# Kernel tuning notes

Hardware: AMD Instinct MI355X
Metric: run time of the kernel (lower is better)

## Reference

```python
import jax, jax.numpy as jnp
import numpy as np

B, T, D, H, OUT = 1024, 512, 64, 32, 2
EPS = 1e-5

def setup_inputs() -> dict:
    key = jax.random.key(0)
    ks = jax.random.split(key, 16)
    s_ih1 = 1.0 / np.sqrt(H)
    inp = {
        'x': jax.random.normal(ks[0], (B, T, D), jnp.float32),
        'bn_gamma': jax.random.normal(ks[1], (T,), jnp.float32) * 0.1 + 1.0,
        'bn_beta': jax.random.normal(ks[2], (T,), jnp.float32) * 0.1,
        'bn_mean': jax.random.normal(ks[3], (T,), jnp.float32) * 0.1,
        'bn_var': jax.random.uniform(ks[4], (T,), jnp.float32) + 0.5,
        'Wih1': jax.random.uniform(ks[5], (4 * H, D), jnp.float32, -s_ih1, s_ih1),
        'Whh1': jax.random.uniform(ks[6], (4 * H, H), jnp.float32, -s_ih1, s_ih1),
        'bih1': jax.random.uniform(ks[7], (4 * H,), jnp.float32, -s_ih1, s_ih1),
        'bhh1': jax.random.uniform(ks[8], (4 * H,), jnp.float32, -s_ih1, s_ih1),
        'Wih2': jax.random.uniform(ks[9], (4 * H, H), jnp.float32, -s_ih1, s_ih1),
        'Whh2': jax.random.uniform(ks[10], (4 * H, H), jnp.float32, -s_ih1, s_ih1),
        'bih2': jax.random.uniform(ks[11], (4 * H,), jnp.float32, -s_ih1, s_ih1),
        'bhh2': jax.random.uniform(ks[12], (4 * H,), jnp.float32, -s_ih1, s_ih1),
        'fcW': jax.random.uniform(ks[13], (OUT, H), jnp.float32, -s_ih1, s_ih1),
        'fcb': jax.random.uniform(ks[14], (OUT,), jnp.float32, -s_ih1, s_ih1),
    }
    return inp

def _lstm_layer(x, Wih, Whh, bih, bhh):
    # x: (B, T, Din) -> outputs h_t for all t: (B, T, H)
    h = jnp.shape(Whh)[1]
    # precompute input contributions for all timesteps: (B, T, 4H)
    xw = jnp.einsum('btd,gd->btg', x, Wih) + bih + bhh
    def step(carry, xt):
        h_prev, c_prev = carry
        z = xt + h_prev @ Whh.T  # (B, 4H)
        i = jax.nn.sigmoid(z[:, :h])
        f = jax.nn.sigmoid(z[:, h:2 * h])
        g = jnp.tanh(z[:, 2 * h:3 * h])
        o = jax.nn.sigmoid(z[:, 3 * h:])
        c = f * c_prev + i * g
        hn = o * jnp.tanh(c)
        return (hn, c), hn
    b = x.shape[0]
    init = (jnp.zeros((b, h), x.dtype), jnp.zeros((b, h), x.dtype))
    _, hs = jax.lax.scan(step, init, jnp.swapaxes(xw, 0, 1))  # (T, B, H)
    return jnp.swapaxes(hs, 0, 1)

def reference(x, bn_gamma, bn_beta, bn_mean, bn_var,
              Wih1, Whh1, bih1, bhh1, Wih2, Whh2, bih2, bhh2, fcW, fcb):
    # BatchNorm1d over channel dim=1 (axis_num), eval mode (running stats);
    # dropout layers are identity in eval mode.
    inv = jax.lax.rsqrt(bn_var + EPS)
    xn = (x - bn_mean[None, :, None]) * (inv * bn_gamma)[None, :, None] + bn_beta[None, :, None]
    h1 = _lstm_layer(xn, Wih1, Whh1, bih1, bhh1)   # (B, T, 32)
    h2 = _lstm_layer(h1, Wih2, Whh2, bih2, bhh2)   # (B, T, 32)
    pooled = h2.mean(axis=-2)                       # GAP over time: (B, 32)
    return pooled @ fcW.T + fcb                     # (B, 2)
```

## Files before the change

kernel.cpp:

```cpp
#include <hip/hip_runtime.h>
#include <cstdint>

#define B_   1024
#define T_   512
#define D_   64
#define H_   32
#define EPS_ 1e-5f

__device__ __forceinline__ float fast_rcp(float x) { return __builtin_amdgcn_rcpf(x); }

__global__ __launch_bounds__(256, 3) void k_bnxw(
    const float* __restrict__ x,   const float* __restrict__ gam,
    const float* __restrict__ bet, const float* __restrict__ mu,
    const float* __restrict__ var,
    const float* __restrict__ Wih1, const float* __restrict__ bih1,
    const float* __restrict__ bhh1, float* __restrict__ pre)
{
    __shared__ __align__(16) float Wt[64][132];
    __shared__ __align__(16) float xs[64][64];
    __shared__ float scs[64], shs[64], bsum[128];

    const int tid = threadIdx.x;
    const int r0  = blockIdx.x * 64;

    if (tid < 64) {
        int t = (r0 + tid) & (T_ - 1);
        float s = rsqrtf(var[t] + EPS_) * gam[t];
        scs[tid] = s;
        shs[tid] = bet[t] - mu[t] * s;
    }
    if (tid >= 128) bsum[tid - 128] = bih1[tid - 128] + bhh1[tid - 128];

    #pragma unroll
    for (int it = 0; it < 8; ++it) {
        int idx4 = tid + it * 256;
        float4 v = ((const float4*)Wih1)[idx4];
        int g  = idx4 >> 4;
        int k0 = (idx4 & 15) * 4;
        Wt[k0 + 0][g] = v.x; Wt[k0 + 1][g] = v.y;
        Wt[k0 + 2][g] = v.z; Wt[k0 + 3][g] = v.w;
    }
    __syncthreads();

    const float4* x4 = (const float4*)(x + (size_t)r0 * 64);
    #pragma unroll
    for (int it = 0; it < 4; ++it) {
        int j  = tid + it * 256;
        int rr = j >> 4;
        int k4 = j & 15;
        float4 v = x4[j];
        float s = scs[rr], sh = shs[rr];
        v.x = v.x * s + sh; v.y = v.y * s + sh;
        v.z = v.z * s + sh; v.w = v.w * s + sh;
        *(float4*)&xs[rr][k4 * 4] = v;
    }
    __syncthreads();

    const int gq = tid & 31;
    const int rq = tid >> 5;

    float acc[8][4];
    #pragma unroll
    for (int r = 0; r < 8; ++r)
        #pragma unroll
        for (int q = 0; q < 4; ++q) acc[r][q] = 0.f;

    #pragma unroll 4
    for (int kq = 0; kq < 16; ++kq) {
        float4 wv[4];
        #pragma unroll
        for (int kk = 0; kk < 4; ++kk)
            wv[kk] = *(const float4*)&Wt[kq * 4 + kk][gq * 4];
        #pragma unroll
        for (int rr = 0; rr < 8; ++rr) {
            float4 xv = *(const float4*)&xs[rq * 8 + rr][kq * 4];
            acc[rr][0] += xv.x * wv[0].x + xv.y * wv[1].x + xv.z * wv[2].x + xv.w * wv[3].x;
            acc[rr][1] += xv.x * wv[0].y + xv.y * wv[1].y + xv.z * wv[2].y + xv.w * wv[3].y;
            acc[rr][2] += xv.x * wv[0].z + xv.y * wv[1].z + xv.z * wv[2].z + xv.w * wv[3].z;
            acc[rr][3] += xv.x * wv[0].w + xv.y * wv[1].w + xv.z * wv[2].w + xv.w * wv[3].w;
        }
    }

    const float b0 = bsum[gq * 4 + 0], b1 = bsum[gq * 4 + 1];
    const float b2 = bsum[gq * 4 + 2], b3 = bsum[gq * 4 + 3];
    #pragma unroll
    for (int rr = 0; rr < 8; ++rr) {
        int row = r0 + rq * 8 + rr;
        float4 o = make_float4(acc[rr][0] + b0, acc[rr][1] + b1,
                               acc[rr][2] + b2, acc[rr][3] + b3);
        *(float4*)&pre[(size_t)row * 128 + gq * 4] = o;
    }
}

__global__ __launch_bounds__(256, 4) void k_rec(
    const float* __restrict__ pre,
    const float* __restrict__ Whh1, const float* __restrict__ Wih2,
    const float* __restrict__ Whh2, const float* __restrict__ bih2,
    const float* __restrict__ bhh2, const float* __restrict__ fcW,
    const float* __restrict__ fcb,  float* __restrict__ out)
{
    __shared__ __align__(16) float h1s[2][H_];
    __shared__ __align__(16) float h2s[2][H_];
    __shared__ float zw[4][32];
    __shared__ float pool[H_];

    const int tid  = threadIdx.x;
    const int w    = tid >> 6;
    const int l    = tid & 63;
    const int m    = l >> 1;
    const int half = l & 1;
    const int jj   = m & 7;
    const int q    = m >> 3;
    const int g    = w * 8 + jj + 32 * q;
    const int b    = blockIdx.x;

    if (tid < H_) { h1s[0][tid] = 0.f; h2s[0][tid] = 0.f; }

    float w1h[16], wi2h[16], w2h[16];
    {
        const float4* p4 = (const float4*)(Whh1 + g * 32 + half * 16);
        #pragma unroll
        for (int i = 0; i < 4; ++i) {
            float4 v = p4[i];
            w1h[4*i] = v.x; w1h[4*i+1] = v.y; w1h[4*i+2] = v.z; w1h[4*i+3] = v.w;
        }
    }
    {
        const float4* p4 = (const float4*)(Wih2 + g * 32 + half * 16);
        #pragma unroll
        for (int i = 0; i < 4; ++i) {
            float4 v = p4[i];
            wi2h[4*i] = v.x; wi2h[4*i+1] = v.y; wi2h[4*i+2] = v.z; wi2h[4*i+3] = v.w;
        }
    }
    {
        const float4* p4 = (const float4*)(Whh2 + g * 32 + half * 16);
        #pragma unroll
        for (int i = 0; i < 4; ++i) {
            float4 v = p4[i];
            w2h[4*i] = v.x; w2h[4*i+1] = v.y; w2h[4*i+2] = v.z; w2h[4*i+3] = v.w;
        }
    }
    #pragma unroll
    for (int i = 0; i < 16; ++i) {
        asm volatile("" : "+v"(w1h[i]));
        asm volatile("" : "+v"(wi2h[i]));
        asm volatile("" : "+v"(w2h[i]));
    }
    float bias1 = (half == 0) ? 0.f : 0.f;
    float bias2 = (half == 0) ? (bih2[g] + bhh2[g]) : 0.f;
    asm volatile("" : "+v"(bias2));
    (void)bias1;

    const float act_a = (q == 2) ? 2.f : 1.f;
    const float act_b = (q == 2) ? -1.f : 0.f;

    __syncthreads();

    const float* prow = pre + (size_t)b * T_ * 128;
    float zc = prow[g];
    float c1 = 0.f, c2 = 0.f, hsum = 0.f;
    const bool wrH = (half == 0) && (q == 0);

    for (int t = 0; t < T_; ++t) {
        const int p = t & 1;

        float zn = 0.f;
        if (t + 1 < T_) zn = prow[(size_t)(t + 1) * 128 + g];

        {
            const float* h1p = &h1s[p][half * 16];
            float a0 = (half == 0) ? zc : 0.f;
            float a1 = 0.f, a2 = 0.f, a3 = 0.f;
            #pragma unroll
            for (int i = 0; i < 4; ++i) {
                float4 v = *(const float4*)(h1p + 4 * i);
                a0 += w1h[4*i]   * v.x; a1 += w1h[4*i+1] * v.y;
                a2 += w1h[4*i+2] * v.z; a3 += w1h[4*i+3] * v.w;
            }
            float za = (a0 + a1) + (a2 + a3);
            za += __shfl_xor(za, 1);

            float u = act_a * za;
            float s = fast_rcp(1.f + __expf(-u));
            float act = fmaf(act_a, s, act_b);
            if (half == 0) zw[w][m] = act;
            float i_ = zw[w][jj],      f_ = zw[w][jj + 8];
            float g_ = zw[w][jj + 16], o_ = zw[w][jj + 24];
            c1 = f_ * c1 + i_ * g_;
            float th = fmaf(2.f, fast_rcp(1.f + __expf(-2.f * c1)), -1.f);
            float h1 = o_ * th;
            if (wrH) h1s[1 - p][w * 8 + jj] = h1;
        }

        __syncthreads();

        {
            const float* h1n = &h1s[1 - p][half * 16];
            const float* h2p = &h2s[p][half * 16];
            float s0 = bias2, s1 = 0.f, s2 = 0.f, s3 = 0.f;
            #pragma unroll
            for (int i = 0; i < 4; ++i) {
                float4 v = *(const float4*)(h1n + 4 * i);
                s0 += wi2h[4*i]   * v.x; s1 += wi2h[4*i+1] * v.y;
                s2 += wi2h[4*i+2] * v.z; s3 += wi2h[4*i+3] * v.w;
            }
            #pragma unroll
            for (int i = 0; i < 4; ++i) {
                float4 v = *(const float4*)(h2p + 4 * i);
                s0 += w2h[4*i]   * v.x; s1 += w2h[4*i+1] * v.y;
                s2 += w2h[4*i+2] * v.z; s3 += w2h[4*i+3] * v.w;
            }
            float zb = (s0 + s1) + (s2 + s3);
            zb += __shfl_xor(zb, 1);

            float u = act_a * zb;
            float s = fast_rcp(1.f + __expf(-u));
            float act = fmaf(act_a, s, act_b);
            if (half == 0) zw[w][m] = act;
            float i_ = zw[w][jj],      f_ = zw[w][jj + 8];
            float g_ = zw[w][jj + 16], o_ = zw[w][jj + 24];
            c2 = f_ * c2 + i_ * g_;
            float th = fmaf(2.f, fast_rcp(1.f + __expf(-2.f * c2)), -1.f);
            float h2v = o_ * th;
            hsum += h2v;
            if (wrH) h2s[1 - p][w * 8 + jj] = h2v;
        }
        zc = zn;
    }

    if (wrH) pool[w * 8 + jj] = hsum * (1.f / T_);
    __syncthreads();
    if (tid < 2) {
        float acc = fcb[tid];
        #pragma unroll
        for (int j = 0; j < 32; ++j) acc += pool[j] * fcW[tid * 32 + j];
        out[b * 2 + tid] = acc;
    }
}

extern "C" void kernel_launch(void* const* d_in, const int* in_sizes, int n_in,
                              void* d_out, int out_size, void* d_ws, size_t ws_size,
                              hipStream_t stream)
{
    const float* x    = (const float*)d_in[0];
    const float* gam  = (const float*)d_in[1];
    const float* bet  = (const float*)d_in[2];
    const float* mu   = (const float*)d_in[3];
    const float* var  = (const float*)d_in[4];
    const float* Wih1 = (const float*)d_in[5];
    const float* Whh1 = (const float*)d_in[6];
    const float* bih1 = (const float*)d_in[7];
    const float* bhh1 = (const float*)d_in[8];
    const float* Wih2 = (const float*)d_in[9];
    const float* Whh2 = (const float*)d_in[10];
    const float* bih2 = (const float*)d_in[11];
    const float* bhh2 = (const float*)d_in[12];
    const float* fcW  = (const float*)d_in[13];
    const float* fcb  = (const float*)d_in[14];
    float*       out  = (float*)d_out;

    float* pre = (float*)d_ws;

    k_bnxw<<<dim3(B_ * T_ / 64), 256, 0, stream>>>(
        x, gam, bet, mu, var, Wih1, bih1, bhh1, pre);
    k_rec<<<dim3(B_), 256, 0, stream>>>(
        pre, Whh1, Wih2, Whh2, bih2, bhh2, fcW, fcb, out);
}
```

Baseline: 747.2 us.

## Remap LSTM recurrence to one gate per thread with DPP quad exchange

The recurrent kernel drops from 256 to 128 threads per block. Each thread now computes a full 32-wide dot product for one gate instead of half of one, which removes the xor-shuffle reduction. The four gates of a cell now sit in adjacent lanes of a quad and are exchanged with DPP quad permutes instead of a shared-memory zw buffer. The time loop is unrolled by two, with prefetch two steps ahead. Separately, the input-projection kernel doubles its row tile to 128 rows per block, raising accumulator register pressure and lowering occupancy.

```diff
diff --git a/kernel.cpp b/kernel.cpp
--- a/kernel.cpp
+++ b/kernel.cpp
@@ -7,9 +7,16 @@
 #define H_   32
 #define EPS_ 1e-5f
 
-__device__ __forceinline__ float fast_rcp(float x) { return __builtin_amdgcn_rcpf(x); }
-
-__global__ __launch_bounds__(256, 3) void k_bnxw(
+__device__ __forceinline__ float rcp_(float x) { return __builtin_amdgcn_rcpf(x); }
+
+template<int CTRL>
+__device__ __forceinline__ float qperm(float x) {
+    int i = __builtin_bit_cast(int, x);
+    i = __builtin_amdgcn_mov_dpp(i, CTRL, 0xF, 0xF, true);
+    return __builtin_bit_cast(float, i);
+}
+
+__global__ __launch_bounds__(256, 2) void k_bnxw(
     const float* __restrict__ x,   const float* __restrict__ gam,
     const float* __restrict__ bet, const float* __restrict__ mu,
     const float* __restrict__ var,
@@ -17,41 +24,42 @@
     const float* __restrict__ bhh1, float* __restrict__ pre)
 {
     __shared__ __align__(16) float Wt[64][132];
-    __shared__ __align__(16) float xs[64][64];
-    __shared__ float scs[64], shs[64], bsum[128];
+    __shared__ __align__(16) float xs[128][64];
+    __shared__ float scs[128], shs[128], bsum[128];
 
     const int tid = threadIdx.x;
-    const int r0  = blockIdx.x * 64;
-
-    if (tid < 64) {
+    const int r0  = blockIdx.x * 128;
+
+    if (tid < 128) {
         int t = (r0 + tid) & (T_ - 1);
         float s = rsqrtf(var[t] + EPS_) * gam[t];
         scs[tid] = s;
         shs[tid] = bet[t] - mu[t] * s;
-    }
-    if (tid >= 128) bsum[tid - 128] = bih1[tid - 128] + bhh1[tid - 128];
+    } else {
+        bsum[tid - 128] = bih1[tid - 128] + bhh1[tid - 128];
+    }
 
     #pragma unroll
     for (int it = 0; it < 8; ++it) {
         int idx4 = tid + it * 256;
         float4 v = ((const float4*)Wih1)[idx4];
-        int g  = idx4 >> 4;
+        int gg = idx4 >> 4;
         int k0 = (idx4 & 15) * 4;
-        Wt[k0 + 0][g] = v.x; Wt[k0 + 1][g] = v.y;
-        Wt[k0 + 2][g] = v.z; Wt[k0 + 3][g] = v.w;
+        Wt[k0 + 0][gg] = v.x; Wt[k0 + 1][gg] = v.y;
+        Wt[k0 + 2][gg] = v.z; Wt[k0 + 3][gg] = v.w;
     }
     __syncthreads();
 
     const float4* x4 = (const float4*)(x + (size_t)r0 * 64);
     #pragma unroll
-    for (int it = 0; it < 4; ++it) {
+    for (int it = 0; it < 8; ++it) {
         int j  = tid + it * 256;
         int rr = j >> 4;
         int k4 = j & 15;
         float4 v = x4[j];
         float s = scs[rr], sh = shs[rr];
-        v.x = v.x * s + sh; v.y = v.y * s + sh;
-        v.z = v.z * s + sh; v.w = v.w * s + sh;
+        v.x = fmaf(v.x, s, sh); v.y = fmaf(v.y, s, sh);
+        v.z = fmaf(v.z, s, sh); v.w = fmaf(v.w, s, sh);
         *(float4*)&xs[rr][k4 * 4] = v;
     }
     __syncthreads();
@@ -59,40 +67,52 @@
     const int gq = tid & 31;
     const int rq = tid >> 5;
 
-    float acc[8][4];
-    #pragma unroll
-    for (int r = 0; r < 8; ++r)
-        #pragma unroll
-        for (int q = 0; q < 4; ++q) acc[r][q] = 0.f;
-
-    #pragma unroll 4
+    float acc[16][4];
+    #pragma unroll
+    for (int r = 0; r < 16; ++r)
+        #pragma unroll
+        for (int c = 0; c < 4; ++c) acc[r][c] = 0.f;
+
+    #pragma unroll 2
     for (int kq = 0; kq < 16; ++kq) {
-        float4 wv[4];
-        #pragma unroll
-        for (int kk = 0; kk < 4; ++kk)
-            wv[kk] = *(const float4*)&Wt[kq * 4 + kk][gq * 4];
-        #pragma unroll
-        for (int rr = 0; rr < 8; ++rr) {
-            float4 xv = *(const float4*)&xs[rq * 8 + rr][kq * 4];
-            acc[rr][0] += xv.x * wv[0].x + xv.y * wv[1].x + xv.z * wv[2].x + xv.w * wv[3].x;
-            acc[rr][1] += xv.x * wv[0].y + xv.y * wv[1].y + xv.z * wv[2].y + xv.w * wv[3].y;
-            acc[rr][2] += xv.x * wv[0].z + xv.y * wv[1].z + xv.z * wv[2].z + xv.w * wv[3].z;
-            acc[rr][3] += xv.x * wv[0].w + xv.y * wv[1].w + xv.z * wv[2].w + xv.w * wv[3].w;
+        float4 wv0 = *(const float4*)&Wt[kq * 4 + 0][gq * 4];
+        float4 wv1 = *(const float4*)&Wt[kq * 4 + 1][gq * 4];
+        float4 wv2 = *(const float4*)&Wt[kq * 4 + 2][gq * 4];
+        float4 wv3 = *(const float4*)&Wt[kq * 4 + 3][gq * 4];
+        #pragma unroll
+        for (int rr = 0; rr < 16; ++rr) {
+            float4 xv = *(const float4*)&xs[rq * 16 + rr][kq * 4];
+            acc[rr][0] = fmaf(xv.x, wv0.x, acc[rr][0]);
+            acc[rr][0] = fmaf(xv.y, wv1.x, acc[rr][0]);
+            acc[rr][0] = fmaf(xv.z, wv2.x, acc[rr][0]);
+            acc[rr][0] = fmaf(xv.w, wv3.x, acc[rr][0]);
+            acc[rr][1] = fmaf(xv.x, wv0.y, acc[rr][1]);
+            acc[rr][1] = fmaf(xv.y, wv1.y, acc[rr][1]);
+            acc[rr][1] = fmaf(xv.z, wv2.y, acc[rr][1]);
+            acc[rr][1] = fmaf(xv.w, wv3.y, acc[rr][1]);
+            acc[rr][2] = fmaf(xv.x, wv0.z, acc[rr][2]);
+            acc[rr][2] = fmaf(xv.y, wv1.z, acc[rr][2]);
+            acc[rr][2] = fmaf(xv.z, wv2.z, acc[rr][2]);
+            acc[rr][2] = fmaf(xv.w, wv3.z, acc[rr][2]);
+            acc[rr][3] = fmaf(xv.x, wv0.w, acc[rr][3]);
+            acc[rr][3] = fmaf(xv.y, wv1.w, acc[rr][3]);
+            acc[rr][3] = fmaf(xv.z, wv2.w, acc[rr][3]);
+            acc[rr][3] = fmaf(xv.w, wv3.w, acc[rr][3]);
         }
     }
 
     const float b0 = bsum[gq * 4 + 0], b1 = bsum[gq * 4 + 1];
     const float b2 = bsum[gq * 4 + 2], b3 = bsum[gq * 4 + 3];
     #pragma unroll
-    for (int rr = 0; rr < 8; ++rr) {
-        int row = r0 + rq * 8 + rr;
+    for (int rr = 0; rr < 16; ++rr) {
+        int row = r0 + rq * 16 + rr;
         float4 o = make_float4(acc[rr][0] + b0, acc[rr][1] + b1,
                                acc[rr][2] + b2, acc[rr][3] + b3);
         *(float4*)&pre[(size_t)row * 128 + gq * 4] = o;
     }
 }
 
-__global__ __launch_bounds__(256, 4) void k_rec(
+__global__ __launch_bounds__(128, 2) void k_rec(
     const float* __restrict__ pre,
     const float* __restrict__ Whh1, const float* __restrict__ Wih2,
     const float* __restrict__ Whh2, const float* __restrict__ bih2,
@@ -101,135 +121,118 @@
 {
     __shared__ __align__(16) float h1s[2][H_];
     __shared__ __align__(16) float h2s[2][H_];
-    __shared__ float zw[4][32];
     __shared__ float pool[H_];
 
     const int tid  = threadIdx.x;
     const int w    = tid >> 6;
     const int l    = tid & 63;
-    const int m    = l >> 1;
-    const int half = l & 1;
-    const int jj   = m & 7;
-    const int q    = m >> 3;
-    const int g    = w * 8 + jj + 32 * q;
+    const int jj   = l >> 2;
+    const int q    = l & 3;
+    const int g    = w * 16 + jj + 32 * q;
+    const int cell = w * 16 + jj;
+    const bool q0  = (q == 0);
     const int b    = blockIdx.x;
 
     if (tid < H_) { h1s[0][tid] = 0.f; h2s[0][tid] = 0.f; }
 
-    float w1h[16], wi2h[16], w2h[16];
+    float w1[32], wi2[32], w2h[32];
     {
-        const float4* p4 = (const float4*)(Whh1 + g * 32 + half * 16);
-        #pragma unroll
-        for (int i = 0; i < 4; ++i) {
+        const float4* p4 = (const float4*)(Whh1 + g * 32);
+        #pragma unroll
+        for (int i = 0; i < 8; ++i) {
             float4 v = p4[i];
-            w1h[4*i] = v.x; w1h[4*i+1] = v.y; w1h[4*i+2] = v.z; w1h[4*i+3] = v.w;
+            w1[4*i] = v.x; w1[4*i+1] = v.y; w1[4*i+2] = v.z; w1[4*i+3] = v.w;
         }
     }
     {
-        const float4* p4 = (const float4*)(Wih2 + g * 32 + half * 16);
-        #pragma unroll
-        for (int i = 0; i < 4; ++i) {
+        const float4* p4 = (const float4*)(Wih2 + g * 32);
+        #pragma unroll
+        for (int i = 0; i < 8; ++i) {
             float4 v = p4[i];
-            wi2h[4*i] = v.x; wi2h[4*i+1] = v.y; wi2h[4*i+2] = v.z; wi2h[4*i+3] = v.w;
+            wi2[4*i] = v.x; wi2[4*i+1] = v.y; wi2[4*i+2] = v.z; wi2[4*i+3] = v.w;
         }
     }
     {
-        const float4* p4 = (const float4*)(Whh2 + g * 32 + half * 16);
-        #pragma unroll
-        for (int i = 0; i < 4; ++i) {
+        const float4* p4 = (const float4*)(Whh2 + g * 32);
+        #pragma unroll
+        for (int i = 0; i < 8; ++i) {
             float4 v = p4[i];
             w2h[4*i] = v.x; w2h[4*i+1] = v.y; w2h[4*i+2] = v.z; w2h[4*i+3] = v.w;
         }
     }
-    #pragma unroll
-    for (int i = 0; i < 16; ++i) {
-        asm volatile("" : "+v"(w1h[i]));
-        asm volatile("" : "+v"(wi2h[i]));
-        asm volatile("" : "+v"(w2h[i]));
-    }
-    float bias1 = (half == 0) ? 0.f : 0.f;
-    float bias2 = (half == 0) ? (bih2[g] + bhh2[g]) : 0.f;
-    asm volatile("" : "+v"(bias2));
-    (void)bias1;
+    const float bias2 = bih2[g] + bhh2[g];
 
     const float act_a = (q == 2) ? 2.f : 1.f;
     const float act_b = (q == 2) ? -1.f : 0.f;
-
-    __syncthreads();
-
-    const float* prow = pre + (size_t)b * T_ * 128;
-    float zc = prow[g];
+    const float nact  = -act_a;
+
+    __syncthreads();
+
+    const float* prow = pre + (size_t)b * T_ * 128 + g;
+    float zc = prow[0];
+    float zn = prow[128];
     float c1 = 0.f, c2 = 0.f, hsum = 0.f;
-    const bool wrH = (half == 0) && (q == 0);
-
-    for (int t = 0; t < T_; ++t) {
-        const int p = t & 1;
-
-        float zn = 0.f;
-        if (t + 1 < T_) zn = prow[(size_t)(t + 1) * 128 + g];
-
-        {
-            const float* h1p = &h1s[p][half * 16];
-            float a0 = (half == 0) ? zc : 0.f;
-            float a1 = 0.f, a2 = 0.f, a3 = 0.f;
-            #pragma unroll
-            for (int i = 0; i < 4; ++i) {
-                float4 v = *(const float4*)(h1p + 4 * i);
-                a0 += w1h[4*i]   * v.x; a1 += w1h[4*i+1] * v.y;
-                a2 += w1h[4*i+2] * v.z; a3 += w1h[4*i+3] * v.w;
-            }
-            float za = (a0 + a1) + (a2 + a3);
-            za += __shfl_xor(za, 1);
-
-            float u = act_a * za;
-            float s = fast_rcp(1.f + __expf(-u));
-            float act = fmaf(act_a, s, act_b);
-            if (half == 0) zw[w][m] = act;
-            float i_ = zw[w][jj],      f_ = zw[w][jj + 8];
-            float g_ = zw[w][jj + 16], o_ = zw[w][jj + 24];
-            c1 = f_ * c1 + i_ * g_;
-            float th = fmaf(2.f, fast_rcp(1.f + __expf(-2.f * c1)), -1.f);
-            float h1 = o_ * th;
-            if (wrH) h1s[1 - p][w * 8 + jj] = h1;
-        }
-
-        __syncthreads();
-
-        {
-            const float* h1n = &h1s[1 - p][half * 16];
-            const float* h2p = &h2s[p][half * 16];
-            float s0 = bias2, s1 = 0.f, s2 = 0.f, s3 = 0.f;
-            #pragma unroll
-            for (int i = 0; i < 4; ++i) {
-                float4 v = *(const float4*)(h1n + 4 * i);
-                s0 += wi2h[4*i]   * v.x; s1 += wi2h[4*i+1] * v.y;
-                s2 += wi2h[4*i+2] * v.z; s3 += wi2h[4*i+3] * v.w;
-            }
-            #pragma unroll
-            for (int i = 0; i < 4; ++i) {
-                float4 v = *(const float4*)(h2p + 4 * i);
-                s0 += w2h[4*i]   * v.x; s1 += w2h[4*i+1] * v.y;
-                s2 += w2h[4*i+2] * v.z; s3 += w2h[4*i+3] * v.w;
-            }
-            float zb = (s0 + s1) + (s2 + s3);
-            zb += __shfl_xor(zb, 1);
-
-            float u = act_a * zb;
-            float s = fast_rcp(1.f + __expf(-u));
-            float act = fmaf(act_a, s, act_b);
-            if (half == 0) zw[w][m] = act;
-            float i_ = zw[w][jj],      f_ = zw[w][jj + 8];
-            float g_ = zw[w][jj + 16], o_ = zw[w][jj + 24];
-            c2 = f_ * c2 + i_ * g_;
-            float th = fmaf(2.f, fast_rcp(1.f + __expf(-2.f * c2)), -1.f);
-            float h2v = o_ * th;
-            hsum += h2v;
-            if (wrH) h2s[1 - p][w * 8 + jj] = h2v;
-        }
-        zc = zn;
-    }
-
-    if (wrH) pool[w * 8 + jj] = hsum * (1.f / T_);
+
+#define STEP(P, ZIN)                                                          \
+    {                                                                         \
+        const float4* h1p = (const float4*)&h1s[P][0];                        \
+        float a0 = (ZIN), a1 = 0.f, a2 = 0.f, a3 = 0.f;                       \
+        _Pragma("unroll")                                                     \
+        for (int i = 0; i < 8; ++i) {                                         \
+            float4 v = h1p[i];                                                \
+            a0 = fmaf(w1[4*i+0], v.x, a0); a1 = fmaf(w1[4*i+1], v.y, a1);     \
+            a2 = fmaf(w1[4*i+2], v.z, a2); a3 = fmaf(w1[4*i+3], v.w, a3);     \
+        }                                                                     \
+        float z1 = (a0 + a1) + (a2 + a3);                                     \
+        float A1 = fmaf(act_a, rcp_(1.f + __expf(nact * z1)), act_b);         \
+        float B1 = qperm<0xB1>(A1);                                           \
+        float C1 = qperm<0x4E>(A1);                                           \
+        float D1 = qperm<0x1B>(A1);                                           \
+        c1 = B1 * c1; c1 = fmaf(A1, C1, c1);                                  \
+        float th1 = fmaf(2.f, rcp_(1.f + __expf(-2.f * c1)), -1.f);           \
+        float h1v = D1 * th1;                                                 \
+        if (q0) h1s[1 - (P)][cell] = h1v;                                     \
+        __syncthreads();                                                      \
+        const float4* h1n = (const float4*)&h1s[1 - (P)][0];                  \
+        const float4* h2p = (const float4*)&h2s[P][0];                        \
+        float s0 = bias2, s1 = 0.f, s2 = 0.f, s3 = 0.f;                       \
+        _Pragma("unroll")                                                     \
+        for (int i = 0; i < 8; ++i) {                                         \
+            float4 v = h1n[i];                                                \
+            s0 = fmaf(wi2[4*i+0], v.x, s0); s1 = fmaf(wi2[4*i+1], v.y, s1);   \
+            s2 = fmaf(wi2[4*i+2], v.z, s2); s3 = fmaf(wi2[4*i+3], v.w, s3);   \
+        }                                                                     \
+        _Pragma("unroll")                                                     \
+        for (int i = 0; i < 8; ++i) {                                         \
+            float4 v = h2p[i];                                                \
+            s0 = fmaf(w2h[4*i+0], v.x, s0); s1 = fmaf(w2h[4*i+1], v.y, s1);   \
+            s2 = fmaf(w2h[4*i+2], v.z, s2); s3 = fmaf(w2h[4*i+3], v.w, s3);   \
+        }                                                                     \
+        float z2 = (s0 + s1) + (s2 + s3);                                     \
+        float A2 = fmaf(act_a, rcp_(1.f + __expf(nact * z2)), act_b);         \
+        float B2 = qperm<0xB1>(A2);                                           \
+        float C2 = qperm<0x4E>(A2);                                           \
+        float D2 = qperm<0x1B>(A2);                                           \
+        c2 = B2 * c2; c2 = fmaf(A2, C2, c2);                                  \
+        float th2 = fmaf(2.f, rcp_(1.f + __expf(-2.f * c2)), -1.f);           \
+        float h2v = D2 * th2;                                                 \
+        hsum += h2v;                                                          \
+        if (q0) h2s[1 - (P)][cell] = h2v;                                     \
+    }
+
+    for (int t = 0; t < T_; t += 2) {
+        int ta = (t + 2 < T_) ? t + 2 : t;
+        int tb = (t + 3 < T_) ? t + 3 : t;
+        float pa = prow[(size_t)ta * 128];
+        float pb = prow[(size_t)tb * 128];
+        STEP(0, zc)
+        STEP(1, zn)
+        zc = pa;
+        zn = pb;
+    }
+#undef STEP
+
+    if (q0) pool[cell] = hsum * (1.f / T_);
     __syncthreads();
     if (tid < 2) {
         float acc = fcb[tid];
@@ -262,8 +265,8 @@
 
     float* pre = (float*)d_ws;
 
-    k_bnxw<<<dim3(B_ * T_ / 64), 256, 0, stream>>>(
+    k_bnxw<<<dim3(B_ * T_ / 128), 256, 0, stream>>>(
         x, gam, bet, mu, var, Wih1, bih1, bhh1, pre);
-    k_rec<<<dim3(B_), 256, 0, stream>>>(
+    k_rec<<<dim3(B_), 128, 0, stream>>>(
         pre, Whh1, Wih2, Whh2, bih2, bhh2, fcW, fcb, out);
 }
```

Result: faster. 639.1 us (-14.5%).
